# Optimization experiments

Measured on AMD Instinct MI355X. Metric: run time of the kernel, lower is better.

## Reference

```python
import jax
import jax.numpy as jnp
import numpy as np

TEMPERATURE = 0.07
NUM_HARD = 4
ALPHA = 2.0
NEG_INF = -1.0e9


def setup_inputs() -> dict:
    key = jax.random.key(0)
    k1, k2 = jax.random.split(key)
    B, D = 8192, 256
    v = jax.random.normal(k1, (B, D), dtype=jnp.float32)
    t = jax.random.normal(k2, (B, D), dtype=jnp.float32)
    # embeddings are assumed unit-norm (cosine similarity in the original module)
    v = v / jnp.linalg.norm(v, axis=-1, keepdims=True)
    t = t / jnp.linalg.norm(t, axis=-1, keepdims=True)
    return {"vision_embed": v, "text_embed": t}


def reference(vision_embed, text_embed):
    B = vision_embed.shape[0]
    rows = jnp.arange(B)
    # [B, B] similarity logits
    sim = jnp.einsum("bd,cd->bc", vision_embed, text_embed) / TEMPERATURE
    # mask diagonal, take top-k hardest negatives per row
    sim_off = sim.at[rows, rows].set(NEG_INF)
    k = min(NUM_HARD, B - 1)
    _, hard_idx = jax.lax.top_k(sim_off, k)  # [B, k]
    # weights: alpha at hard negatives, 1 elsewhere (diag forced to 1)
    weights = jnp.ones_like(sim)
    weights = weights.at[rows[:, None], hard_idx].set(ALPHA)
    weights = weights.at[rows, rows].set(1.0)
    sw = sim * weights  # weighted logits, shared by both directions
    # v->t: row softmax; t->v: sim.T * weights.T == sw.T -> column softmax of sw
    logp_v2t = jax.nn.log_softmax(sw, axis=1)
    logp_t2v = jax.nn.log_softmax(sw, axis=0)
    loss_v2t = -jnp.mean(logp_v2t[rows, rows])
    loss_t2v = -jnp.mean(logp_t2v[rows, rows])
    return (loss_v2t + loss_t2v) / 2.0
```

## Files before the change

### kernel.cpp

```cpp
#include <hip/hip_runtime.h>
#include <hip/hip_bf16.h>
#include <math.h>

#define B_SIZE 8192
#define D_SIZE 256
#define INV_T 14.285714285714286f

typedef __bf16 bf16x8 __attribute__((ext_vector_type(8)));
typedef float f32x4 __attribute__((ext_vector_type(4)));

__device__ __forceinline__ void gload_lds16(const void* g, void* lds) {
  __builtin_amdgcn_global_load_lds(
      (const __attribute__((address_space(1))) void*)g,
      (__attribute__((address_space(3))) void*)lds, 16, 0, 0);
}

__device__ __forceinline__ void ce(float& av, int& ai, float& bv, int& bi) {
  const bool sw = av < bv;
  const float hv = sw ? bv : av;  const int hidx = sw ? bi : ai;
  const float lv = sw ? av : bv;  const int lidx = sw ? ai : bi;
  av = hv; ai = hidx; bv = lv; bi = lidx;
}

__device__ __forceinline__ void merge_top4(float a[4], int ai[4],
                                           float b[4], int bi[4]) {
  ce(a[0], ai[0], b[3], bi[3]);
  ce(a[1], ai[1], b[2], bi[2]);
  ce(a[2], ai[2], b[1], bi[1]);
  ce(a[3], ai[3], b[0], bi[0]);
  ce(a[0], ai[0], a[2], ai[2]);
  ce(a[1], ai[1], a[3], ai[3]);
  ce(a[0], ai[0], a[1], ai[1]);
  ce(a[2], ai[2], a[3], ai[3]);
}

__global__ __launch_bounds__(256) void cvt_bf16_kernel(
    const float* __restrict__ in, __hip_bfloat16* __restrict__ out,
    float scale, int n4) {
  int i = blockIdx.x * 256 + threadIdx.x;
  if (i >= n4) return;
  const float4 v = reinterpret_cast<const float4*>(in)[i];
  union { __hip_bfloat16 h[4]; short4 s; } u;
  u.h[0] = __float2bfloat16(v.x * scale);
  u.h[1] = __float2bfloat16(v.y * scale);
  u.h[2] = __float2bfloat16(v.z * scale);
  u.h[3] = __float2bfloat16(v.w * scale);
  reinterpret_cast<short4*>(out)[i] = u.s;
}

__global__ __launch_bounds__(256) void gemm_analyze(
    const __hip_bfloat16* __restrict__ Vb, const __hip_bfloat16* __restrict__ Tb,
    float* __restrict__ row_sum, float* __restrict__ col_sum,
    float* __restrict__ diag,
    float* __restrict__ cand_val, int* __restrict__ cand_idx) {
  __shared__ __align__(16) char smem[33792];
  __shared__ float rsum[128];
  __shared__ float csum[128];

  const int tid  = threadIdx.x;
  const int wave = tid >> 6;
  const int lane = tid & 63;
  const int tileRow = blockIdx.x >> 6;
  const int tileCol = blockIdx.x & 63;
  const int wr = wave >> 1;
  const int wc = wave & 1;
  const int g = lane >> 4;
  const int frow = lane & 15;
  const int rsw = frow & 7;

  __hip_bfloat16* As = reinterpret_cast<__hip_bfloat16*>(smem);
  __hip_bfloat16* Bs = As + 128 * 64;

  if (tid < 128) rsum[tid] = 0.f; else csum[tid - 128] = 0.f;

  f32x4 acc[4][4];
#pragma unroll
  for (int m = 0; m < 4; ++m)
#pragma unroll
    for (int n = 0; n < 4; ++n)
      acc[m][n] = f32x4{0.f, 0.f, 0.f, 0.f};

  const int srow = wave * 32 + (lane >> 3);
  const int scol = ((lane & 7) ^ ((lane >> 3) & 7)) * 8;
  const __hip_bfloat16* Ag = Vb + (size_t)(tileRow * 128 + srow) * D_SIZE + scol;
  const __hip_bfloat16* Bg = Tb + (size_t)(tileCol * 128 + srow) * D_SIZE + scol;
  char* AsStage = (char*)As + wave * 4096;
  char* BsStage = (char*)Bs + wave * 4096;

  for (int k0 = 0; k0 < D_SIZE; k0 += 64) {
#pragma unroll
    for (int i = 0; i < 4; ++i) {
      gload_lds16(Ag + (size_t)i * 8 * D_SIZE + k0, AsStage + i * 1024);
      gload_lds16(Bg + (size_t)i * 8 * D_SIZE + k0, BsStage + i * 1024);
    }
    __syncthreads();
#pragma unroll
    for (int ks = 0; ks < 64; ks += 32) {
      const int cbase = (ks >> 3) + g;
      const int coff = ((cbase ^ rsw) << 4);
      bf16x8 tf[4], vf[4];
#pragma unroll
      for (int n = 0; n < 4; ++n)
        tf[n] = *reinterpret_cast<const bf16x8*>(
            (const char*)Bs + (wc * 64 + n * 16 + frow) * 128 + coff);
#pragma unroll
      for (int m = 0; m < 4; ++m)
        vf[m] = *reinterpret_cast<const bf16x8*>(
            (const char*)As + (wr * 64 + m * 16 + frow) * 128 + coff);
#pragma unroll
      for (int m = 0; m < 4; ++m)
#pragma unroll
        for (int n = 0; n < 4; ++n)
          acc[m][n] = __builtin_amdgcn_mfma_f32_16x16x32_bf16(
              tf[n], vf[m], acc[m][n], 0, 0, 0);
    }
    __syncthreads();
  }

  float* candV = reinterpret_cast<float*>(smem);
  int*   candI = reinterpret_cast<int*>(smem + 16896);

  const bool diagT = (tileRow == tileCol) && (wr == wc);
  const int rowBase = tileRow * 128 + wr * 64;
  const int colBase = tileCol * 128 + wc * 64 + g * 4;

  float cp[16];
#pragma unroll
  for (int k = 0; k < 16; ++k) cp[k] = 0.f;

#pragma unroll
  for (int m = 0; m < 4; ++m) {
    float rs = 0.f;
    float t0v = -3e38f, t1v = -3e38f, t2v = -3e38f, t3v = -3e38f;
    int t0i = 0, t1i = 0, t2i = 0, t3i = 0;
#pragma unroll
    for (int n = 0; n < 4; ++n) {
#pragma unroll
      for (int r = 0; r < 4; ++r) {
        const float v = acc[m][n][r];
        const float e = __expf(v);
        rs += e;
        cp[n * 4 + r] += e;
        const bool isDiag = diagT && (n == m) && ((g * 4 + r) == frow);
        if (isDiag) diag[rowBase + m * 16 + frow] = v;
        const float vt = isDiag ? -3e38f : v;
        const int ci = colBase + n * 16 + r;
        const bool b0 = vt > t0v, b1 = vt > t1v, b2 = vt > t2v, b3 = vt > t3v;
        t3v = b2 ? t2v : (b3 ? vt : t3v);  t3i = b2 ? t2i : (b3 ? ci : t3i);
        t2v = b1 ? t1v : (b2 ? vt : t2v);  t2i = b1 ? t1i : (b2 ? ci : t2i);
        t1v = b0 ? t0v : (b1 ? vt : t1v);  t1i = b0 ? t0i : (b1 ? ci : t1i);
        t0v = b0 ? vt : t0v;               t0i = b0 ? ci : t0i;
      }
    }
    rs += __shfl_xor(rs, 16);
    rs += __shfl_xor(rs, 32);
    if (g == 0) atomicAdd(&rsum[wr * 64 + m * 16 + frow], rs);
    const int cb = (wr * 64 + m * 16 + frow) * 33 + (wc * 4 + g) * 4;
    candV[cb + 0] = t0v; candV[cb + 1] = t1v;
    candV[cb + 2] = t2v; candV[cb + 3] = t3v;
    candI[cb + 0] = t0i; candI[cb + 1] = t1i;
    candI[cb + 2] = t2i; candI[cb + 3] = t3i;
  }

#pragma unroll
  for (int s = 8; s >= 1; s >>= 1) {
    const bool up = (lane & s) != 0;
#pragma unroll
    for (int k = 0; k < 8; ++k) {
      if (k < s) {
        const float send = up ? cp[k] : cp[k + s];
        const float recv = __shfl_xor(send, s);
        cp[k] = (up ? cp[k + s] : cp[k]) + recv;
      }
    }
  }
  atomicAdd(&csum[wc * 64 + ((frow >> 2) << 4) + (g << 2) + (frow & 3)], cp[0]);

  __syncthreads();

  if (tid < 128) {
    const int row = tid;
    const int base = row * 33;
    float av[4]; int ai[4];
#pragma unroll
    for (int k = 0; k < 4; ++k) { av[k] = candV[base + k]; ai[k] = candI[base + k]; }
#pragma unroll
    for (int l = 1; l < 8; ++l) {
      float bv[4]; int bi[4];
#pragma unroll
      for (int k = 0; k < 4; ++k) {
        bv[k] = candV[base + l * 4 + k];
        bi[k] = candI[base + l * 4 + k];
      }
      merge_top4(av, ai, bv, bi);
    }
    const int gRow = tileRow * 128 + row;
    const size_t cb = ((size_t)gRow << 8) + (tileCol << 2);
    float4 v4; v4.x = av[0]; v4.y = av[1]; v4.z = av[2]; v4.w = av[3];
    int4 i4; i4.x = ai[0]; i4.y = ai[1]; i4.z = ai[2]; i4.w = ai[3];
    *reinterpret_cast<float4*>(cand_val + cb) = v4;
    *reinterpret_cast<int4*>(cand_idx + cb) = i4;
    atomicAdd(&row_sum[gRow], rsum[row]);
  } else {
    const int c = tid - 128;
    atomicAdd(&col_sum[tileCol * 128 + c], csum[c]);
  }
}

__global__ __launch_bounds__(256) void merge_correct(
    const float* __restrict__ cand_val, const int* __restrict__ cand_idx,
    float* __restrict__ row_sum, float* __restrict__ col_sum) {
  const int wave = threadIdx.x >> 6;
  const int lane = threadIdx.x & 63;
  const int row = blockIdx.x * 4 + wave;

  const size_t base = ((size_t)row << 8) + lane * 4;
  const float4 v4 = *reinterpret_cast<const float4*>(cand_val + base);
  const int4 i4 = *reinterpret_cast<const int4*>(cand_idx + base);
  float v[4] = {v4.x, v4.y, v4.z, v4.w};
  int   id[4] = {i4.x, i4.y, i4.z, i4.w};

#pragma unroll
  for (int s = 1; s < 64; s <<= 1) {
    float bv[4]; int bi[4];
#pragma unroll
    for (int k = 0; k < 4; ++k) {
      bv[k] = __shfl_xor(v[k], s);
      bi[k] = __shfl_xor(id[k], s);
    }
    merge_top4(v, id, bv, bi);
  }

  if (lane == 0) {
    float corr = 0.f;
#pragma unroll
    for (int k = 0; k < 4; ++k) {
      const float e1 = __expf(v[k]);
      const float e2 = __expf(2.f * v[k]);
      const float c = e2 - e1;
      corr += c;
      atomicAdd(&col_sum[id[k]], c);
    }
    row_sum[row] += corr;
  }
}

__global__ __launch_bounds__(256) void finalize(
    const float* __restrict__ row_sum, const float* __restrict__ col_sum,
    const float* __restrict__ diag, float* __restrict__ out) {
  double s = 0.0;
  for (int i = threadIdx.x; i < B_SIZE; i += 256)
    s += (double)(logf(row_sum[i]) + logf(col_sum[i]) - 2.f * diag[i]);
#pragma unroll
  for (int d = 1; d < 64; d <<= 1) s += __shfl_xor(s, d);
  __shared__ double red[4];
  const int lane = threadIdx.x & 63, wave = threadIdx.x >> 6;
  if (lane == 0) red[wave] = s;
  __syncthreads();
  if (threadIdx.x == 0) {
    const double tot = red[0] + red[1] + red[2] + red[3];
    out[0] = (float)(tot / (2.0 * (double)B_SIZE));
  }
}

extern "C" void kernel_launch(void* const* d_in, const int* in_sizes, int n_in,
                              void* d_out, int out_size, void* d_ws, size_t ws_size,
                              hipStream_t stream) {
  const float* V = (const float*)d_in[0];
  const float* T = (const float*)d_in[1];
  float* out = (float*)d_out;
  char* ws = (char*)d_ws;

  __hip_bfloat16* Vb = (__hip_bfloat16*)ws;
  __hip_bfloat16* Tb = (__hip_bfloat16*)(ws + (4 << 20));
  float* row_sum = (float*)(ws + (8 << 20));
  float* col_sum = row_sum + B_SIZE;
  float* diag    = col_sum + B_SIZE;
  float* cand_val = (float*)(ws + (8 << 20) + 3 * B_SIZE * 4);
  int*   cand_idx = (int*)((char*)cand_val + (8 << 20));

  hipMemsetAsync(row_sum, 0, 2 * B_SIZE * sizeof(float), stream);

  const int n4 = B_SIZE * D_SIZE / 4;
  cvt_bf16_kernel<<<n4 / 256, 256, 0, stream>>>(V, Vb, INV_T, n4);
  cvt_bf16_kernel<<<n4 / 256, 256, 0, stream>>>(T, Tb, 1.0f, n4);

  gemm_analyze<<<64 * 64, 256, 0, stream>>>(Vb, Tb, row_sum, col_sum, diag,
                                            cand_val, cand_idx);
  merge_correct<<<B_SIZE / 4, 256, 0, stream>>>(cand_val, cand_idx,
                                                row_sum, col_sum);
  finalize<<<1, 256, 0, stream>>>(row_sum, col_sum, diag, out);
}
```

Measured before the change: 196.2 us.

## Pack top-k candidates into sortable int keys and fold log2e into scaling

Top-k candidates are now single 32-bit keys: the float logit's upper bits combined with the 13-bit column index. This lets the top-k tracking use integer max/min, and each lane keeps only its top 2 per 16 columns instead of top 4, which halves shared and global candidate traffic. Logits are pre-scaled by log2e so exp2f replaces expf. The two conversion kernels and the memset are merged into one launch. The key truncates the low mantissa bits, so near-ties may rank differently and the correction uses rounded values, which risks small accuracy differences.

```diff
diff --git a/kernel.cpp b/kernel.cpp
--- a/kernel.cpp
+++ b/kernel.cpp
@@ -5,6 +5,10 @@
 #define B_SIZE 8192
 #define D_SIZE 256
 #define INV_T 14.285714285714286f
+#define LOG2E 1.4426950408889634f
+#define LN2 0.6931471805599453f
+#define KEY_MASK 0xFFFFE000
+#define COL_MASK 0x1FFF
 
 typedef __bf16 bf16x8 __attribute__((ext_vector_type(8)));
 typedef float f32x4 __attribute__((ext_vector_type(4)));
@@ -15,45 +19,44 @@
       (__attribute__((address_space(3))) void*)lds, 16, 0, 0);
 }
 
-__device__ __forceinline__ void ce(float& av, int& ai, float& bv, int& bi) {
-  const bool sw = av < bv;
-  const float hv = sw ? bv : av;  const int hidx = sw ? bi : ai;
-  const float lv = sw ? av : bv;  const int lidx = sw ? ai : bi;
-  av = hv; ai = hidx; bv = lv; bi = lidx;
-}
-
-__device__ __forceinline__ void merge_top4(float a[4], int ai[4],
-                                           float b[4], int bi[4]) {
-  ce(a[0], ai[0], b[3], bi[3]);
-  ce(a[1], ai[1], b[2], bi[2]);
-  ce(a[2], ai[2], b[1], bi[1]);
-  ce(a[3], ai[3], b[0], bi[0]);
-  ce(a[0], ai[0], a[2], ai[2]);
-  ce(a[1], ai[1], a[3], ai[3]);
-  ce(a[0], ai[0], a[1], ai[1]);
-  ce(a[2], ai[2], a[3], ai[3]);
-}
-
-__global__ __launch_bounds__(256) void cvt_bf16_kernel(
-    const float* __restrict__ in, __hip_bfloat16* __restrict__ out,
-    float scale, int n4) {
-  int i = blockIdx.x * 256 + threadIdx.x;
-  if (i >= n4) return;
-  const float4 v = reinterpret_cast<const float4*>(in)[i];
+__device__ __forceinline__ void cei(int& a, int& b) {
+  const int h = a > b ? a : b;
+  const int l = a > b ? b : a;
+  a = h; b = l;
+}
+
+__device__ __forceinline__ void merge_top4i(int a[4], int b[4]) {
+  cei(a[0], b[3]); cei(a[1], b[2]); cei(a[2], b[1]); cei(a[3], b[0]);
+  cei(a[0], a[2]); cei(a[1], a[3]); cei(a[0], a[1]); cei(a[2], a[3]);
+}
+
+__global__ __launch_bounds__(256) void cvt_both(
+    const float* __restrict__ V, const float* __restrict__ T,
+    __hip_bfloat16* __restrict__ Vb, __hip_bfloat16* __restrict__ Tb,
+    float* __restrict__ sums) {
+  const int b = blockIdx.x;
+  if (b < 16)
+    reinterpret_cast<float4*>(sums)[b * 256 + threadIdx.x] =
+        float4{0.f, 0.f, 0.f, 0.f};
+  const int half = b >> 11;
+  const int i = (b & 2047) * 256 + threadIdx.x;
+  const float sc = half ? 1.0f : (INV_T * LOG2E);
+  const float* src = half ? T : V;
+  __hip_bfloat16* dst = half ? Tb : Vb;
+  const float4 v = reinterpret_cast<const float4*>(src)[i];
   union { __hip_bfloat16 h[4]; short4 s; } u;
-  u.h[0] = __float2bfloat16(v.x * scale);
-  u.h[1] = __float2bfloat16(v.y * scale);
-  u.h[2] = __float2bfloat16(v.z * scale);
-  u.h[3] = __float2bfloat16(v.w * scale);
-  reinterpret_cast<short4*>(out)[i] = u.s;
+  u.h[0] = __float2bfloat16(v.x * sc);
+  u.h[1] = __float2bfloat16(v.y * sc);
+  u.h[2] = __float2bfloat16(v.z * sc);
+  u.h[3] = __float2bfloat16(v.w * sc);
+  reinterpret_cast<short4*>(dst)[i] = u.s;
 }
 
 __global__ __launch_bounds__(256) void gemm_analyze(
     const __hip_bfloat16* __restrict__ Vb, const __hip_bfloat16* __restrict__ Tb,
     float* __restrict__ row_sum, float* __restrict__ col_sum,
-    float* __restrict__ diag,
-    float* __restrict__ cand_val, int* __restrict__ cand_idx) {
-  __shared__ __align__(16) char smem[33792];
+    float* __restrict__ diag, int* __restrict__ cand_key) {
+  __shared__ __align__(16) char smem[32768];
   __shared__ float rsum[128];
   __shared__ float csum[128];
 
@@ -117,12 +120,12 @@
     __syncthreads();
   }
 
-  float* candV = reinterpret_cast<float*>(smem);
-  int*   candI = reinterpret_cast<int*>(smem + 16896);
+  int* candK = reinterpret_cast<int*>(smem);
 
   const bool diagT = (tileRow == tileCol) && (wr == wc);
+  const bool diagLane = diagT && (g == (frow >> 2));
   const int rowBase = tileRow * 128 + wr * 64;
-  const int colBase = tileCol * 128 + wc * 64 + g * 4;
+  const int colOr = tileCol * 128 + wc * 64 + g * 4;
 
   float cp[16];
 #pragma unroll
@@ -131,35 +134,35 @@
 #pragma unroll
   for (int m = 0; m < 4; ++m) {
     float rs = 0.f;
-    float t0v = -3e38f, t1v = -3e38f, t2v = -3e38f, t3v = -3e38f;
-    int t0i = 0, t1i = 0, t2i = 0, t3i = 0;
+    int t0 = (int)0x80000000, t1 = (int)0x80000000;
 #pragma unroll
     for (int n = 0; n < 4; ++n) {
 #pragma unroll
       for (int r = 0; r < 4; ++r) {
-        const float v = acc[m][n][r];
-        const float e = __expf(v);
+        const float a = acc[m][n][r];
+        const float e = exp2f(a);
         rs += e;
         cp[n * 4 + r] += e;
-        const bool isDiag = diagT && (n == m) && ((g * 4 + r) == frow);
-        if (isDiag) diag[rowBase + m * 16 + frow] = v;
-        const float vt = isDiag ? -3e38f : v;
-        const int ci = colBase + n * 16 + r;
-        const bool b0 = vt > t0v, b1 = vt > t1v, b2 = vt > t2v, b3 = vt > t3v;
-        t3v = b2 ? t2v : (b3 ? vt : t3v);  t3i = b2 ? t2i : (b3 ? ci : t3i);
-        t2v = b1 ? t1v : (b2 ? vt : t2v);  t2i = b1 ? t1i : (b2 ? ci : t2i);
-        t1v = b0 ? t0v : (b1 ? vt : t1v);  t1i = b0 ? t0i : (b1 ? ci : t1i);
-        t0v = b0 ? vt : t0v;               t0i = b0 ? ci : t0i;
+        const int key =
+            ((__float_as_int(a) & KEY_MASK) | colOr) | (n * 16 + r);
+        t1 = max(t1, min(t0, key));
+        t0 = max(t0, key);
       }
     }
     rs += __shfl_xor(rs, 16);
     rs += __shfl_xor(rs, 32);
     if (g == 0) atomicAdd(&rsum[wr * 64 + m * 16 + frow], rs);
-    const int cb = (wr * 64 + m * 16 + frow) * 33 + (wc * 4 + g) * 4;
-    candV[cb + 0] = t0v; candV[cb + 1] = t1v;
-    candV[cb + 2] = t2v; candV[cb + 3] = t3v;
-    candI[cb + 0] = t0i; candI[cb + 1] = t1i;
-    candI[cb + 2] = t2i; candI[cb + 3] = t3i;
+    if (diagLane) {
+      const int rr = frow & 3;
+      float dv = acc[m][m][0];
+      dv = rr == 1 ? acc[m][m][1] : dv;
+      dv = rr == 2 ? acc[m][m][2] : dv;
+      dv = rr == 3 ? acc[m][m][3] : dv;
+      diag[rowBase + m * 16 + frow] = dv * LN2;
+      t0 = t1; t1 = (int)0x80000000;
+    }
+    const int cb = (wr * 64 + m * 16 + frow) * 17 + (wc * 4 + g) * 2;
+    candK[cb] = t0; candK[cb + 1] = t1;
   }
 
 #pragma unroll
@@ -180,26 +183,18 @@
 
   if (tid < 128) {
     const int row = tid;
-    const int base = row * 33;
-    float av[4]; int ai[4];
-#pragma unroll
-    for (int k = 0; k < 4; ++k) { av[k] = candV[base + k]; ai[k] = candI[base + k]; }
+    const int base = row * 17;
+    int a[4] = {candK[base], candK[base + 1], (int)0x80000000, (int)0x80000000};
 #pragma unroll
     for (int l = 1; l < 8; ++l) {
-      float bv[4]; int bi[4];
-#pragma unroll
-      for (int k = 0; k < 4; ++k) {
-        bv[k] = candV[base + l * 4 + k];
-        bi[k] = candI[base + l * 4 + k];
-      }
-      merge_top4(av, ai, bv, bi);
+      int b[4] = {candK[base + l * 2], candK[base + l * 2 + 1],
+                  (int)0x80000000, (int)0x80000000};
+      merge_top4i(a, b);
     }
     const int gRow = tileRow * 128 + row;
     const size_t cb = ((size_t)gRow << 8) + (tileCol << 2);
-    float4 v4; v4.x = av[0]; v4.y = av[1]; v4.z = av[2]; v4.w = av[3];
-    int4 i4; i4.x = ai[0]; i4.y = ai[1]; i4.z = ai[2]; i4.w = ai[3];
-    *reinterpret_cast<float4*>(cand_val + cb) = v4;
-    *reinterpret_cast<int4*>(cand_idx + cb) = i4;
+    int4 o; o.x = a[0]; o.y = a[1]; o.z = a[2]; o.w = a[3];
+    *reinterpret_cast<int4*>(cand_key + cb) = o;
     atomicAdd(&row_sum[gRow], rsum[row]);
   } else {
     const int c = tid - 128;
@@ -208,38 +203,32 @@
 }
 
 __global__ __launch_bounds__(256) void merge_correct(
-    const float* __restrict__ cand_val, const int* __restrict__ cand_idx,
+    const int* __restrict__ cand_key,
     float* __restrict__ row_sum, float* __restrict__ col_sum) {
   const int wave = threadIdx.x >> 6;
   const int lane = threadIdx.x & 63;
   const int row = blockIdx.x * 4 + wave;
 
-  const size_t base = ((size_t)row << 8) + lane * 4;
-  const float4 v4 = *reinterpret_cast<const float4*>(cand_val + base);
-  const int4 i4 = *reinterpret_cast<const int4*>(cand_idx + base);
-  float v[4] = {v4.x, v4.y, v4.z, v4.w};
-  int   id[4] = {i4.x, i4.y, i4.z, i4.w};
+  const int4 k4 = *reinterpret_cast<const int4*>(
+      cand_key + ((size_t)row << 8) + lane * 4);
+  int v[4] = {k4.x, k4.y, k4.z, k4.w};
 
 #pragma unroll
   for (int s = 1; s < 64; s <<= 1) {
-    float bv[4]; int bi[4];
-#pragma unroll
-    for (int k = 0; k < 4; ++k) {
-      bv[k] = __shfl_xor(v[k], s);
-      bi[k] = __shfl_xor(id[k], s);
-    }
-    merge_top4(v, id, bv, bi);
+    int b[4];
+#pragma unroll
+    for (int k = 0; k < 4; ++k) b[k] = __shfl_xor(v[k], s);
+    merge_top4i(v, b);
   }
 
   if (lane == 0) {
     float corr = 0.f;
 #pragma unroll
     for (int k = 0; k < 4; ++k) {
-      const float e1 = __expf(v[k]);
-      const float e2 = __expf(2.f * v[k]);
-      const float c = e2 - e1;
+      const float a = __int_as_float(v[k] & KEY_MASK);
+      const float c = exp2f(a + a) - exp2f(a);
       corr += c;
-      atomicAdd(&col_sum[id[k]], c);
+      atomicAdd(&col_sum[v[k] & COL_MASK], c);
     }
     row_sum[row] += corr;
   }
@@ -276,18 +265,11 @@
   float* row_sum = (float*)(ws + (8 << 20));
   float* col_sum = row_sum + B_SIZE;
   float* diag    = col_sum + B_SIZE;
-  float* cand_val = (float*)(ws + (8 << 20) + 3 * B_SIZE * 4);
-  int*   cand_idx = (int*)((char*)cand_val + (8 << 20));
-
-  hipMemsetAsync(row_sum, 0, 2 * B_SIZE * sizeof(float), stream);
-
-  const int n4 = B_SIZE * D_SIZE / 4;
-  cvt_bf16_kernel<<<n4 / 256, 256, 0, stream>>>(V, Vb, INV_T, n4);
-  cvt_bf16_kernel<<<n4 / 256, 256, 0, stream>>>(T, Tb, 1.0f, n4);
-
+  int*   cand_key = (int*)(ws + (8 << 20) + 3 * B_SIZE * 4);
+
+  cvt_both<<<4096, 256, 0, stream>>>(V, T, Vb, Tb, row_sum);
   gemm_analyze<<<64 * 64, 256, 0, stream>>>(Vb, Tb, row_sum, col_sum, diag,
-                                            cand_val, cand_idx);
-  merge_correct<<<B_SIZE / 4, 256, 0, stream>>>(cand_val, cand_idx,
-                                                row_sum, col_sum);
+                                            cand_key);
+  merge_correct<<<B_SIZE / 4, 256, 0, stream>>>(cand_key, row_sum, col_sum);
   finalize<<<1, 256, 0, stream>>>(row_sum, col_sum, diag, out);
 }
```

Result: faster. 170.0 us (-13.4%).
